# Kernel tuning notes

Measured on AMD Instinct MI355X. Metric: run time of the kernel, lower is better.

Reference implementation:

```python
import jax, jax.numpy as jnp
import numpy as np
from jax import lax

N, K = 4, 8
B, C, H, W = 16, 64, 256, 256


def setup_inputs() -> dict:
    key = jax.random.key(0)
    k1, k2, k3 = jax.random.split(key, 3)
    x = jax.random.normal(k1, (B, C, H, W), dtype=jnp.float32)
    z = jax.random.normal(k2, (B, C, N * K, N * K), dtype=jnp.float32)
    # torch init is ones; perturb slightly so the FFT filtering is non-trivial
    freq_coeff = 1.0 + 0.1 * jax.random.normal(k3, (K, K // 2 + 1, 2), dtype=jnp.float32)
    return {"x": x, "z": z, "freq_coeff": freq_coeff}


def _get_feature_weights(z, freq_coeff, n, k):
    b, c = z.shape[0], z.shape[1]
    # [b,c,n,k,n,k] -> [b,n,n,c,k,k] -> [b*n*n, c, k, k]
    w1 = z.reshape(b, c, n, k, n, k).transpose(0, 2, 4, 1, 3, 5).reshape(b * n * n, c, k, k)
    f = jnp.fft.rfft2(w1, norm="ortho")  # [b*n*n, c, k, k//2+1] complex
    # torch.rfft(..)*freq_coeff multiplies real/imag parts by separate real coeffs
    f_new = f.real * freq_coeff[..., 0] + 1j * (f.imag * freq_coeff[..., 1])
    return jnp.fft.irfft2(f_new, s=(k, k), norm="ortho")  # [b*n*n, c, k, k]


def _grouped_conv(data, weight, b):
    # data: [1, b*c, h, w], weight: [b*n*n, c, k, k], groups=b, stride 2, VALID
    return lax.conv_general_dilated(
        data, weight, window_strides=(2, 2), padding="VALID",
        dimension_numbers=("NCHW", "OIHW", "NCHW"), feature_group_count=b)


def reference(x, z, freq_coeff):
    k = freq_coeff.shape[0]
    n = z.shape[2] // k
    b, c, h, w = x.shape
    weight = _get_feature_weights(z, freq_coeff, n, k)
    data = x.reshape(1, b * c, h, w)
    resp = _grouped_conv(data, weight, b)  # [1, b*n*n, h', w']
    norm = _grouped_conv(data * data, jnp.ones_like(weight), b)
    norm = norm + jnp.std(norm, ddof=1) / 10 + 1e-9
    norm = lax.stop_gradient(0.01 / jnp.sqrt(norm))
    resp = resp * norm
    _, cc, hh, ww = resp.shape
    return resp.reshape(b, cc // b, hh, ww)
```

## Files before the change

kernel.cpp:

```cpp
#include <hip/hip_runtime.h>

typedef short short8 __attribute__((ext_vector_type(8)));
typedef float f32x4 __attribute__((ext_vector_type(4)));
typedef unsigned int uint4v __attribute__((ext_vector_type(4)));

static constexpr int OHW = 125;
static constexpr int PLN = OHW * OHW;

__device__ inline unsigned int bf16_rne(float f) {
  unsigned int u = __float_as_uint(f);
  return (u + 0x7FFFu + ((u >> 16) & 1u)) >> 16;
}

__global__ __launch_bounds__(256) void fft_mat_kernel(
    const float* __restrict__ fc, float* __restrict__ Mt, double* __restrict__ red) {
  if (blockIdx.x == 0 && threadIdx.x < 2) red[threadIdx.x] = 0.0;
  int e = blockIdx.x * 256 + threadIdx.x;
  int uv = e >> 6, xy = e & 63;
  int u = uv >> 3, v = uv & 7, xx = xy >> 3, yy = xy & 7;
  const float R2 = 0.70710678118654752f;
  const float ct[8] = {1.f, R2, 0.f, -R2, -1.f, -R2, 0.f, R2};
  const float st[8] = {0.f, R2, 1.f, R2, 0.f, -R2, -1.f, -R2};
  float sumv = 0.f;
  #pragma unroll
  for (int p = 0; p < 8; ++p) {
    #pragma unroll
    for (int q = 0; q < 8; ++q) {
      float Re, Im;
      if (q <= 4) {
        int th = (p * u + q * v) & 7;
        float a = fc[(p * 5 + q) * 2 + 0];
        float b = fc[(p * 5 + q) * 2 + 1];
        Re = a * ct[th];
        Im = -b * st[th];
      } else {
        int pp = (8 - p) & 7, qq = 8 - q;
        int th = (pp * u + qq * v) & 7;
        float a = fc[(pp * 5 + qq) * 2 + 0];
        float b = fc[(pp * 5 + qq) * 2 + 1];
        Re = a * ct[th];
        Im = b * st[th];
      }
      int ph = (p * xx + q * yy) & 7;
      sumv += Re * ct[ph] - Im * st[ph];
    }
  }
  Mt[e] = sumv * (1.0f / 64.0f);
}

__global__ __launch_bounds__(256) void weight_kernel(
    const float* __restrict__ z, const float* __restrict__ Mt,
    unsigned short* __restrict__ Wq) {
  int blk = blockIdx.x;
  int G = blk >> 2, cq = blk & 3;
  int b = G >> 4, n1 = (G >> 2) & 3, n2 = G & 3;
  int oc = G & 15;
  int tid = threadIdx.x;
  int cs = tid >> 6, xy = tid & 63;
  __shared__ float Ms[4096];
  __shared__ float zb[4][64];
  for (int i = tid; i < 4096; i += 256) Ms[i] = Mt[i];
  for (int it = 0; it < 4; ++it) {
    int c = cq * 16 + cs * 4 + it;
    __syncthreads();
    int u = xy >> 3, vv = xy & 7;
    zb[cs][xy] = z[(size_t)(b * 64 + c) * 1024 + (n1 * 8 + u) * 32 + (n2 * 8 + vv)];
    __syncthreads();
    float acc = 0.f;
    #pragma unroll
    for (int i = 0; i < 64; ++i) acc += Ms[i * 64 + xy] * zb[cs][i];
    Wq[((size_t)(b * 64 + c) * 16 + oc) * 64 + xy] = (unsigned short)bf16_rne(acc);
  }
}

static constexpr int SROWS = 38;
static constexpr int SC4   = 34;
static constexpr int LDW   = 72;
static constexpr int LBUF  = SROWS * LDW;

__global__ __launch_bounds__(1024, 4) void conv_fused_kernel(
    const float* __restrict__ x, const unsigned short* __restrict__ Wq,
    float* __restrict__ resp, float* __restrict__ plane, double* __restrict__ red) {
  __shared__ unsigned int ldsx[2 * LBUF];
  const int g = blockIdx.x, iblk = blockIdx.y, jh = blockIdx.z;
  const int i0 = iblk * 16;
  const int tid = threadIdx.x;
  const int lane = tid & 63, ri = tid >> 6;
  const int q = lane >> 4, n = lane & 15;

  const float* xg = x + (size_t)g * 64 * 65536;
  const unsigned short* wgc = Wq + (size_t)g * 65536;

  int it_goff[2], it_l[2];
  bool it_act[2];
  #pragma unroll
  for (int s = 0; s < 2; ++s) {
    int item = tid + (s << 10);
    int row = item / SC4, c4 = item - row * SC4;
    it_act[s] = row < SROWS;
    int rabs = 2 * i0 + row; if (rabs > 255) rabs = 255;
    int cabs = 128 * jh + 4 * c4; if (cabs > 252) cabs = 252;
    it_goff[s] = rabs * 256 + cabs;
    it_l[s] = row * LDW + 2 * c4;
  }
  const int aoff0 = n * 64 + q * 8;
  int dbase[2];
  #pragma unroll
  for (int h = 0; h < 2; ++h)
    dbase[h] = (2 * ri + q + 4 * h) * LDW + n;

  f32x4 acc[4];
  #pragma unroll
  for (int t = 0; t < 4; ++t) acc[t] = (f32x4){0.f, 0.f, 0.f, 0.f};
  float racc[2][2] = {{0.f, 0.f}, {0.f, 0.f}};

  f32x4 xv[2];
  short8 a_cur[2], a_nxt[2];

  #pragma unroll
  for (int s = 0; s < 2; ++s)
    if (it_act[s]) xv[s] = *(const f32x4*)(xg + it_goff[s]);
  #pragma unroll
  for (int h = 0; h < 2; ++h)
    a_cur[h] = *(const short8*)(wgc + aoff0 + 32 * h);
  #pragma unroll
  for (int s = 0; s < 2; ++s) {
    if (it_act[s]) {
      racc[s][0] += xv[s][0] * xv[s][0] + xv[s][1] * xv[s][1];
      racc[s][1] += xv[s][2] * xv[s][2] + xv[s][3] * xv[s][3];
      unsigned int p0 = bf16_rne(xv[s][0]) | (bf16_rne(xv[s][1]) << 16);
      unsigned int p1 = bf16_rne(xv[s][2]) | (bf16_rne(xv[s][3]) << 16);
      ldsx[it_l[s]] = p0;
      ldsx[it_l[s] + 1] = p1;
    }
  }
  #pragma unroll
  for (int s = 0; s < 2; ++s)
    if (it_act[s]) xv[s] = *(const f32x4*)(xg + 65536 + it_goff[s]);
  #pragma unroll
  for (int h = 0; h < 2; ++h)
    a_nxt[h] = *(const short8*)(wgc + 1024 + aoff0 + 32 * h);
  __syncthreads();

  for (int c = 0; c < 64; ++c) {
    int cb = c & 1;
    if (c < 63) {
      int bo = ((c + 1) & 1) * LBUF;
      #pragma unroll
      for (int s = 0; s < 2; ++s) {
        if (it_act[s]) {
          racc[s][0] += xv[s][0] * xv[s][0] + xv[s][1] * xv[s][1];
          racc[s][1] += xv[s][2] * xv[s][2] + xv[s][3] * xv[s][3];
          unsigned int p0 = bf16_rne(xv[s][0]) | (bf16_rne(xv[s][1]) << 16);
          unsigned int p1 = bf16_rne(xv[s][2]) | (bf16_rne(xv[s][3]) << 16);
          ldsx[bo + it_l[s]] = p0;
          ldsx[bo + it_l[s] + 1] = p1;
        }
      }
      if (c < 62) {
        const float* xc = xg + (size_t)(c + 2) * 65536;
        #pragma unroll
        for (int s = 0; s < 2; ++s)
          if (it_act[s]) xv[s] = *(const f32x4*)(xc + it_goff[s]);
      }
    }
    const unsigned int* xb = ldsx + cb * LBUF;
    #pragma unroll
    for (int h = 0; h < 2; ++h) {
      short8 af = a_cur[h];
      int base = dbase[h];
      #pragma unroll
      for (int T = 0; T < 4; ++T) {
        int d = base + 16 * T;
        uint4v u;
        u.x = xb[d]; u.y = xb[d + 1]; u.z = xb[d + 2]; u.w = xb[d + 3];
        short8 bf = __builtin_bit_cast(short8, u);
        acc[T] = __builtin_amdgcn_mfma_f32_16x16x32_bf16(af, bf, acc[T], 0, 0, 0);
      }
    }
    a_cur[0] = a_nxt[0];
    a_cur[1] = a_nxt[1];
    if (c < 62) {
      const unsigned short* wc = wgc + (size_t)(c + 2) * 1024;
      #pragma unroll
      for (int h = 0; h < 2; ++h)
        a_nxt[h] = *(const short8*)(wc + aoff0 + 32 * h);
    }
    __syncthreads();
  }

  const int i = i0 + ri;
  if (i < OHW) {
    float* rbase = resp + (size_t)g * 16 * PLN + i * OHW;
    #pragma unroll
    for (int T = 0; T < 4; ++T) {
      int j = jh * 64 + T * 16 + n;
      if (j < OHW) {
        #pragma unroll
        for (int r = 0; r < 4; ++r) {
          int oc = q * 4 + r;
          rbase[(size_t)oc * PLN + j] = acc[T][r];
        }
      }
    }
  }

  float* Rl = (float*)ldsx;
  #pragma unroll
  for (int s = 0; s < 2; ++s) {
    if (it_act[s]) {
      Rl[it_l[s]] = racc[s][0];
      Rl[it_l[s] + 1] = racc[s][1];
    }
  }
  __syncthreads();

  int jl = lane;
  float nv = 0.f;
  #pragma unroll
  for (int r = 0; r < 8; ++r) {
    const float* Rr = Rl + (2 * ri + r) * LDW + jl;
    nv += Rr[0] + Rr[1] + Rr[2] + Rr[3];
  }
  int jj = jh * 64 + jl;
  double sv = 0.0, sv2 = 0.0;
  if (i < OHW && jj < OHW) {
    plane[(g * OHW + i) * OHW + jj] = nv;
    sv = (double)nv;
    sv2 = (double)nv * (double)nv;
  }
  #pragma unroll
  for (int off = 32; off > 0; off >>= 1) {
    sv += __shfl_down(sv, off);
    sv2 += __shfl_down(sv2, off);
  }
  __shared__ double sred[32];
  if (lane == 0) { sred[ri] = sv; sred[16 + ri] = sv2; }
  __syncthreads();
  if (tid == 0) {
    double a = 0.0;
    #pragma unroll
    for (int w = 0; w < 16; ++w) a += sred[w];
    atomicAdd(&red[0], a);
  }
  if (tid == 64) {
    double a = 0.0;
    #pragma unroll
    for (int w = 0; w < 16; ++w) a += sred[16 + w];
    atomicAdd(&red[1], a);
  }
}

__global__ void finalize_kernel(const double* __restrict__ red, float* __restrict__ shiftp) {
  double sum = red[0], sumsq = red[1];
  double n = 256.0 * OHW * OHW;
  double mu = 16.0 * sum / n;
  double var = (16.0 * sumsq - n * mu * mu) / (n - 1.0);
  *shiftp = (float)(sqrt(var) / 10.0 + 1e-9);
}

__global__ __launch_bounds__(256) void scale_kernel(
    const float* __restrict__ resp, const float* __restrict__ plane,
    const float* __restrict__ shiftp, float* __restrict__ out) {
  int t = blockIdx.x * 256 + threadIdx.x;
  int idx0 = t * 4;
  if (idx0 >= 16 * 16 * PLN) return;
  float shift = *shiftp;
  int gp = idx0 / (16 * PLN);
  int rem = idx0 - gp * (16 * PLN);
  int ij0 = rem % PLN;
  f32x4 r = *(const f32x4*)(resp + idx0);
  const float* pl = plane + (size_t)gp * PLN;
  f32x4 o;
  #pragma unroll
  for (int k = 0; k < 4; ++k) {
    int ij = ij0 + k; if (ij >= PLN) ij -= PLN;
    o[k] = r[k] * 0.01f * rsqrtf(pl[ij] + shift);
  }
  *(f32x4*)(out + idx0) = o;
}

extern "C" void kernel_launch(void* const* d_in, const int* in_sizes, int n_in,
                              void* d_out, int out_size, void* d_ws, size_t ws_size,
                              hipStream_t stream) {
  const float* x  = (const float*)d_in[0];
  const float* z  = (const float*)d_in[1];
  const float* fc = (const float*)d_in[2];
  float* out = (float*)d_out;

  char* ws = (char*)d_ws;
  unsigned short* Wq = (unsigned short*)(ws);
  float*  Mt     = (float*)(ws + 2097152);
  float*  resp   = (float*)(ws + 2113536);
  float*  plane  = (float*)(ws + 18113536);
  double* red    = (double*)(ws + 19113536);
  float*  shiftp = (float*)(ws + 19113552);

  fft_mat_kernel<<<16, 256, 0, stream>>>(fc, Mt, red);
  weight_kernel<<<1024, 256, 0, stream>>>(z, Mt, Wq);
  conv_fused_kernel<<<dim3(16, 8, 2), 1024, 0, stream>>>(x, Wq, resp, plane, red);
  finalize_kernel<<<1, 1, 0, stream>>>(red, shiftp);
  scale_kernel<<<(16 * 16 * PLN / 4 + 255) / 256, 256, 0, stream>>>(resp, plane, shiftp, out);
}
```

Before: 393.2 us.

## Fuse normalization and scaling into conv kernel via cooperative grid sync

```diff
diff --git a/kernel.cpp b/kernel.cpp
--- a/kernel.cpp
+++ b/kernel.cpp
@@ -1,4 +1,7 @@
 #include <hip/hip_runtime.h>
+#include <hip/hip_cooperative_groups.h>
+
+namespace cg = cooperative_groups;
 
 typedef short short8 __attribute__((ext_vector_type(8)));
 typedef float f32x4 __attribute__((ext_vector_type(4)));
@@ -80,7 +83,7 @@
 
 __global__ __launch_bounds__(1024, 4) void conv_fused_kernel(
     const float* __restrict__ x, const unsigned short* __restrict__ Wq,
-    float* __restrict__ resp, float* __restrict__ plane, double* __restrict__ red) {
+    float* __restrict__ out, double* __restrict__ red) {
   __shared__ unsigned int ldsx[2 * LBUF];
   const int g = blockIdx.x, iblk = blockIdx.y, jh = blockIdx.z;
   const int i0 = iblk * 16;
@@ -189,22 +192,6 @@
     __syncthreads();
   }
 
-  const int i = i0 + ri;
-  if (i < OHW) {
-    float* rbase = resp + (size_t)g * 16 * PLN + i * OHW;
-    #pragma unroll
-    for (int T = 0; T < 4; ++T) {
-      int j = jh * 64 + T * 16 + n;
-      if (j < OHW) {
-        #pragma unroll
-        for (int r = 0; r < 4; ++r) {
-          int oc = q * 4 + r;
-          rbase[(size_t)oc * PLN + j] = acc[T][r];
-        }
-      }
-    }
-  }
-
   float* Rl = (float*)ldsx;
   #pragma unroll
   for (int s = 0; s < 2; ++s) {
@@ -222,10 +209,10 @@
     const float* Rr = Rl + (2 * ri + r) * LDW + jl;
     nv += Rr[0] + Rr[1] + Rr[2] + Rr[3];
   }
+  const int i = i0 + ri;
   int jj = jh * 64 + jl;
   double sv = 0.0, sv2 = 0.0;
   if (i < OHW && jj < OHW) {
-    plane[(g * OHW + i) * OHW + jj] = nv;
     sv = (double)nv;
     sv2 = (double)nv * (double)nv;
   }
@@ -249,35 +236,38 @@
     for (int w = 0; w < 16; ++w) a += sred[16 + w];
     atomicAdd(&red[1], a);
   }
-}
-
-__global__ void finalize_kernel(const double* __restrict__ red, float* __restrict__ shiftp) {
-  double sum = red[0], sumsq = red[1];
-  double n = 256.0 * OHW * OHW;
-  double mu = 16.0 * sum / n;
-  double var = (16.0 * sumsq - n * mu * mu) / (n - 1.0);
-  *shiftp = (float)(sqrt(var) / 10.0 + 1e-9);
-}
-
-__global__ __launch_bounds__(256) void scale_kernel(
-    const float* __restrict__ resp, const float* __restrict__ plane,
-    const float* __restrict__ shiftp, float* __restrict__ out) {
-  int t = blockIdx.x * 256 + threadIdx.x;
-  int idx0 = t * 4;
-  if (idx0 >= 16 * 16 * PLN) return;
-  float shift = *shiftp;
-  int gp = idx0 / (16 * PLN);
-  int rem = idx0 - gp * (16 * PLN);
-  int ij0 = rem % PLN;
-  f32x4 r = *(const f32x4*)(resp + idx0);
-  const float* pl = plane + (size_t)gp * PLN;
-  f32x4 o;
-  #pragma unroll
-  for (int k = 0; k < 4; ++k) {
-    int ij = ij0 + k; if (ij >= PLN) ij -= PLN;
-    o[k] = r[k] * 0.01f * rsqrtf(pl[ij] + shift);
-  }
-  *(f32x4*)(out + idx0) = o;
+  float* pl_l = (float*)ldsx;
+  pl_l[ri * 64 + jl] = nv;
+
+  cg::this_grid().sync();
+
+  __shared__ float s_shift;
+  if (tid == 0) {
+    double sum   = __hip_atomic_load(&red[0], __ATOMIC_RELAXED, __HIP_MEMORY_SCOPE_AGENT);
+    double sumsq = __hip_atomic_load(&red[1], __ATOMIC_RELAXED, __HIP_MEMORY_SCOPE_AGENT);
+    double nn = 256.0 * OHW * OHW;
+    double mu = 16.0 * sum / nn;
+    double var = (16.0 * sumsq - nn * mu * mu) / (nn - 1.0);
+    s_shift = (float)(sqrt(var) / 10.0 + 1e-9);
+  }
+  __syncthreads();
+  const float shift = s_shift;
+
+  if (i < OHW) {
+    float* obase = out + (size_t)g * 16 * PLN + i * OHW;
+    #pragma unroll
+    for (int T = 0; T < 4; ++T) {
+      int j = jh * 64 + T * 16 + n;
+      if (j < OHW) {
+        float sc = 0.01f * rsqrtf(pl_l[ri * 64 + T * 16 + n] + shift);
+        #pragma unroll
+        for (int r = 0; r < 4; ++r) {
+          int oc = q * 4 + r;
+          obase[(size_t)oc * PLN + j] = acc[T][r] * sc;
+        }
+      }
+    }
+  }
 }
 
 extern "C" void kernel_launch(void* const* d_in, const int* in_sizes, int n_in,
@@ -291,14 +281,12 @@
   char* ws = (char*)d_ws;
   unsigned short* Wq = (unsigned short*)(ws);
   float*  Mt     = (float*)(ws + 2097152);
-  float*  resp   = (float*)(ws + 2113536);
-  float*  plane  = (float*)(ws + 18113536);
-  double* red    = (double*)(ws + 19113536);
-  float*  shiftp = (float*)(ws + 19113552);
+  double* red    = (double*)(ws + 2113536);
 
   fft_mat_kernel<<<16, 256, 0, stream>>>(fc, Mt, red);
   weight_kernel<<<1024, 256, 0, stream>>>(z, Mt, Wq);
-  conv_fused_kernel<<<dim3(16, 8, 2), 1024, 0, stream>>>(x, Wq, resp, plane, red);
-  finalize_kernel<<<1, 1, 0, stream>>>(red, shiftp);
-  scale_kernel<<<(16 * 16 * PLN / 4 + 255) / 256, 256, 0, stream>>>(resp, plane, shiftp, out);
-}
+
+  void* args[] = {(void*)&x, (void*)&Wq, (void*)&out, (void*)&red};
+  hipLaunchCooperativeKernel((void*)conv_fused_kernel, dim3(16, 8, 2),
+                             dim3(1024, 1, 1), args, 0, stream);
+}
```

New measurement: 421.0 us. +7.1%, slower.
